# Kernel tuning notes

Hardware: AMD Instinct MI355X
Metric: run time of the kernel (lower is better)

## Reference

```python
import jax, jax.numpy as jnp
import numpy as np

VOCAB = 4096
CODE_DIM = 3


def setup_inputs() -> dict:
    key = jax.random.key(0)
    k1, k2 = jax.random.split(key)
    B, L = 4, 16384
    feats = jax.random.normal(k1, (B, L, CODE_DIM), dtype=jnp.float32)
    # xavier_uniform init for the (vocab, code_dim) embedding table
    limit = float(np.sqrt(6.0 / (VOCAB + CODE_DIM)))
    codebook = jax.random.uniform(k2, (VOCAB, CODE_DIM), dtype=jnp.float32,
                                  minval=-limit, maxval=limit)
    return {"feats": feats, "codebook": codebook}


def reference(feats, codebook):
    """EMAVQ.forward (eval mode): cdist -> argmin -> gather -> vq loss -> straight-through."""
    B, L, D = feats.shape
    flat = feats.reshape(-1, D)                      # (N, D)
    dist = (jnp.sum(flat * flat, axis=1, keepdims=True)
            - 2.0 * (flat @ codebook.T)
            + jnp.sum(codebook * codebook, axis=1))  # (N, V)
    idx = jnp.argmin(dist, axis=1)                   # (N,)
    quant = codebook[idx].reshape(B, L, D)           # embedding gather
    sg = jax.lax.stop_gradient
    loss = (jnp.mean((quant - sg(feats)) ** 2)
            + 0.25 * jnp.mean((feats - sg(quant)) ** 2))
    quant_st = feats + sg(quant - feats)             # straight-through estimator
    return quant_st, idx.reshape(B, L), loss
```

## Files before the change

### kernel.cpp

```cpp
#include <hip/hip_runtime.h>

#define VOCAB 4096
#define SLICES 8
#define SLICE 512
#define GRP 8
#define NGRP (SLICE / GRP)

__device__ __forceinline__ float opaque(float x) {
  asm volatile("" : "+v"(x));
  return x;
}

__device__ __forceinline__ float max3f(float a, float b, float c) {
  float d;
  asm("v_max3_f32 %0, %1, %2, %3" : "=v"(d) : "v"(a), "v"(b), "v"(c));
  return d;
}

__global__ __launch_bounds__(256) void vq_prep_kernel(
    const float* __restrict__ cb, float4* __restrict__ cw,
    float* __restrict__ loss_slot) {
  int j = blockIdx.x * 256 + threadIdx.x;
  if (j == 0) *loss_slot = 0.0f;
  if (j < VOCAB) {
    float e0 = cb[3 * j + 0];
    float e1 = cb[3 * j + 1];
    float e2 = cb[3 * j + 2];
    float p0 = opaque(e0 * e0);
    float p1 = opaque(e1 * e1);
    float p2 = opaque(e2 * e2);
    float c = opaque(opaque(p0 + p1) + p2);
    cw[j] = make_float4(e0, e1, e2, -0.5f * c);
  }
}

__device__ __forceinline__ float tval(float x0, float x1, float x2,
                                      float4 cd) {
  return fmaf(x0, cd.x, fmaf(x1, cd.y, fmaf(x2, cd.z, cd.w)));
}

__device__ __forceinline__ float dist_f32(float x0, float x1, float x2,
                                          float a, float4 cd) {
  float m = fmaf(x2, cd.z, fmaf(x1, cd.y, x0 * cd.x));
  return fmaf(-2.0f, m, a) + (-2.0f * cd.w);
}

__global__ __launch_bounds__(512) void vq_kernel(
    const float* __restrict__ feats, const float4* __restrict__ cw,
    float* __restrict__ out_quant, float* __restrict__ out_idx,
    float* __restrict__ out_loss, int npts) {
  __shared__ float sT1[512];
  __shared__ float sT2[512];
  __shared__ int sG[512];
  __shared__ unsigned long long sSlot[64];
  __shared__ int sList[64];
  __shared__ int sCount;
  __shared__ double sL[64];

  const int tid = threadIdx.x;
  const int lane = tid & 63;
  const int s = __builtin_amdgcn_readfirstlane(tid >> 6);
  const int p = blockIdx.x * 64 + lane;

  if (tid == 0) sCount = 0;

  const float x0 = feats[3 * p + 0];
  const float x1 = feats[3 * p + 1];
  const float x2 = feats[3 * p + 2];

  float xp0 = opaque(x0 * x0);
  float xp1 = opaque(x1 * x1);
  float xp2 = opaque(x2 * x2);
  const float a = opaque(opaque(xp0 + xp1) + xp2);

  const float4* cs = cw + s * SLICE;

  float t1 = -3.4e38f, t2 = -3.4e38f;
  int g1 = 0;
#pragma unroll 2
  for (int g = 0; g < NGRP; ++g) {
    const float4* gp = cs + g * GRP;
    float u0 = tval(x0, x1, x2, gp[0]);
    float u1 = tval(x0, x1, x2, gp[1]);
    float u2 = tval(x0, x1, x2, gp[2]);
    float u3 = tval(x0, x1, x2, gp[3]);
    float u4 = tval(x0, x1, x2, gp[4]);
    float u5 = tval(x0, x1, x2, gp[5]);
    float u6 = tval(x0, x1, x2, gp[6]);
    float u7 = tval(x0, x1, x2, gp[7]);
    float gm = max3f(max3f(u0, u1, u2), max3f(u3, u4, u5), fmaxf(u6, u7));
    t2 = fmaxf(t2, fminf(t1, gm));
    if (gm > t1) g1 = g;
    t1 = fmaxf(t1, gm);
  }
  sT1[tid] = t1;
  sT2[tid] = t2;
  sG[tid] = s * SLICE + g1 * GRP;
  __syncthreads();

  int bi = 0;
  float q0 = 0.0f, q1 = 0.0f, q2 = 0.0f;
  bool flagged = false;
  if (tid < 64) {
    int gbase = sG[tid];
#pragma unroll
    for (int k = 1; k < SLICES; ++k) {
      float b1 = sT1[tid + 64 * k];
      float b2 = sT2[tid + 64 * k];
      t2 = fmaxf(fmaxf(t2, b2), fminf(t1, b1));
      if (b1 > t1) gbase = sG[tid + 64 * k];
      t1 = fmaxf(t1, b1);
    }
    float eps = fmaf(a, 0x1p-21f, 0x1p-20f);
    flagged = !((t1 - t2) > eps);
    if (flagged) {
      int pos = atomicAdd(&sCount, 1);
      sList[pos] = lane;
      sSlot[lane] = ~0ULL;
    } else {
      float bd = 3.4e38f;
#pragma unroll
      for (int k = 0; k < GRP; ++k) {
        float4 cd = cw[gbase + k];
        float d = dist_f32(x0, x1, x2, a, cd);
        if (d < bd) { bd = d; bi = gbase + k; q0 = cd.x; q1 = cd.y; q2 = cd.z; }
      }
    }
  }
  __syncthreads();

  const int cnt = sCount;
  for (int f = 0; f < cnt; ++f) {
    const int fl = sList[f];
    const int fp = blockIdx.x * 64 + fl;
    float y0 = feats[3 * fp + 0];
    float y1 = feats[3 * fp + 1];
    float y2 = feats[3 * fp + 2];
    float yp0 = opaque(y0 * y0);
    float yp1 = opaque(y1 * y1);
    float yp2 = opaque(y2 * y2);
    float ay = opaque(opaque(yp0 + yp1) + yp2);
    float bd = 3.4e38f;
    int bj = 0;
#pragma unroll
    for (int k = 0; k < 8; ++k) {
      float4 cd = cw[tid * 8 + k];
      float d = dist_f32(y0, y1, y2, ay, cd);
      if (d < bd) { bd = d; bj = tid * 8 + k; }
    }
    unsigned b = __float_as_uint(bd);
    b = (b & 0x80000000u) ? ~b : (b | 0x80000000u);
    unsigned long long key = ((unsigned long long)b << 32) | (unsigned)bj;
#pragma unroll
    for (int off = 1; off < 64; off <<= 1) {
      unsigned long long o = __shfl_xor(key, off);
      key = (o < key) ? o : key;
    }
    if (lane == 0) atomicMin(&sSlot[fl], key);
  }
  __syncthreads();

  if (tid < 64) {
    if (flagged) {
      bi = (int)(unsigned)(sSlot[lane] & 0xFFFFFFFFu);
      float4 cd = cw[bi];
      q0 = cd.x; q1 = cd.y; q2 = cd.z;
    }
    float t0 = q0 - x0, t1d = q1 - x1, t2d = q2 - x2;
    out_quant[3 * p + 0] = x0 + t0;
    out_quant[3 * p + 1] = x1 + t1d;
    out_quant[3 * p + 2] = x2 + t2d;
    out_idx[p] = (float)bi;
    sL[lane] = (double)t0 * t0 + (double)t1d * t1d + (double)t2d * t2d;
  }
  __syncthreads();

  if (tid == 0) {
    double acc = 0.0;
#pragma unroll 8
    for (int k = 0; k < 64; ++k) acc += sL[k];
    atomicAdd(out_loss, (float)(acc * (1.25 / ((double)npts * 3.0))));
  }
}

extern "C" void kernel_launch(void* const* d_in, const int* in_sizes, int n_in,
                              void* d_out, int out_size, void* d_ws,
                              size_t ws_size, hipStream_t stream) {
  const float* feats = (const float*)d_in[0];
  const float* cb = (const float*)d_in[1];
  const int npts = in_sizes[0] / 3;

  float* out = (float*)d_out;
  float* out_quant = out;
  float* out_idx = out + in_sizes[0];
  float* out_loss = out + in_sizes[0] + npts;

  float4* cw = (float4*)d_ws;

  vq_prep_kernel<<<VOCAB / 256, 256, 0, stream>>>(cb, cw, out_loss);
  vq_kernel<<<npts / 64, 512, 0, stream>>>(feats, cw, out_quant, out_idx,
                                           out_loss, npts);
}
```

Measured before the change: 108.1 us.

## Stage codebook in LDS and process two points per thread

Each block now copies the whole 4096-entry prepared codebook into shared memory and handles 128 points instead of 64. Every thread scores two points against its codebook slice, so each loaded code entry is reused twice. The aim is to cut codebook fetch and load-issue cost per distance evaluation. In exchange, each block needs about 80KB of LDS, which limits how many blocks fit on a CU, and pays a full codebook copy per block. The wave index is no longer forced to a scalar, so code reads move from scalar loads to LDS broadcast reads.

```diff
diff --git a/kernel.cpp b/kernel.cpp
--- a/kernel.cpp
+++ b/kernel.cpp
@@ -5,6 +5,7 @@
 #define SLICE 512
 #define GRP 8
 #define NGRP (SLICE / GRP)
+#define PTS 128
 
 __device__ __forceinline__ float opaque(float x) {
   asm volatile("" : "+v"(x));
@@ -49,74 +50,100 @@
     const float* __restrict__ feats, const float4* __restrict__ cw,
     float* __restrict__ out_quant, float* __restrict__ out_idx,
     float* __restrict__ out_loss, int npts) {
-  __shared__ float sT1[512];
-  __shared__ float sT2[512];
-  __shared__ int sG[512];
-  __shared__ unsigned long long sSlot[64];
-  __shared__ int sList[64];
+  __shared__ float4 sTab[VOCAB];
+  __shared__ float sT1[SLICES * PTS];
+  __shared__ float sT2[SLICES * PTS];
+  __shared__ int sG[SLICES * PTS];
+  __shared__ unsigned long long sSlot[PTS];
+  __shared__ int sList[PTS];
   __shared__ int sCount;
-  __shared__ double sL[64];
+  __shared__ double sL[PTS];
 
   const int tid = threadIdx.x;
   const int lane = tid & 63;
-  const int s = __builtin_amdgcn_readfirstlane(tid >> 6);
-  const int p = blockIdx.x * 64 + lane;
+  const int s = tid >> 6;
 
   if (tid == 0) sCount = 0;
 
-  const float x0 = feats[3 * p + 0];
-  const float x1 = feats[3 * p + 1];
-  const float x2 = feats[3 * p + 2];
-
-  float xp0 = opaque(x0 * x0);
-  float xp1 = opaque(x1 * x1);
-  float xp2 = opaque(x2 * x2);
-  const float a = opaque(opaque(xp0 + xp1) + xp2);
-
-  const float4* cs = cw + s * SLICE;
-
-  float t1 = -3.4e38f, t2 = -3.4e38f;
-  int g1 = 0;
+#pragma unroll
+  for (int k = 0; k < VOCAB / 512; ++k) sTab[tid + k * 512] = cw[tid + k * 512];
+
+  const int pbase = blockIdx.x * PTS;
+  const int pA = pbase + lane;
+  const int pB = pbase + 64 + lane;
+
+  const float a0 = feats[3 * pA + 0], a1 = feats[3 * pA + 1],
+              a2 = feats[3 * pA + 2];
+  const float b0 = feats[3 * pB + 0], b1 = feats[3 * pB + 1],
+              b2 = feats[3 * pB + 2];
+
+  float ap0 = opaque(a0 * a0), ap1 = opaque(a1 * a1), ap2 = opaque(a2 * a2);
+  const float na = opaque(opaque(ap0 + ap1) + ap2);
+  float bp0 = opaque(b0 * b0), bp1 = opaque(b1 * b1), bp2 = opaque(b2 * b2);
+  const float nb = opaque(opaque(bp0 + bp1) + bp2);
+
+  __syncthreads();
+
+  const float4* cs = sTab + s * SLICE;
+
+  float t1A = -3.4e38f, t2A = -3.4e38f, t1B = -3.4e38f, t2B = -3.4e38f;
+  int gA = 0, gB = 0;
 #pragma unroll 2
   for (int g = 0; g < NGRP; ++g) {
     const float4* gp = cs + g * GRP;
-    float u0 = tval(x0, x1, x2, gp[0]);
-    float u1 = tval(x0, x1, x2, gp[1]);
-    float u2 = tval(x0, x1, x2, gp[2]);
-    float u3 = tval(x0, x1, x2, gp[3]);
-    float u4 = tval(x0, x1, x2, gp[4]);
-    float u5 = tval(x0, x1, x2, gp[5]);
-    float u6 = tval(x0, x1, x2, gp[6]);
-    float u7 = tval(x0, x1, x2, gp[7]);
-    float gm = max3f(max3f(u0, u1, u2), max3f(u3, u4, u5), fmaxf(u6, u7));
-    t2 = fmaxf(t2, fminf(t1, gm));
-    if (gm > t1) g1 = g;
-    t1 = fmaxf(t1, gm);
-  }
-  sT1[tid] = t1;
-  sT2[tid] = t2;
-  sG[tid] = s * SLICE + g1 * GRP;
+    float4 c0 = gp[0], c1 = gp[1], c2 = gp[2], c3 = gp[3];
+    float4 c4 = gp[4], c5 = gp[5], c6 = gp[6], c7 = gp[7];
+    float uA0 = tval(a0, a1, a2, c0), uB0 = tval(b0, b1, b2, c0);
+    float uA1 = tval(a0, a1, a2, c1), uB1 = tval(b0, b1, b2, c1);
+    float uA2 = tval(a0, a1, a2, c2), uB2 = tval(b0, b1, b2, c2);
+    float uA3 = tval(a0, a1, a2, c3), uB3 = tval(b0, b1, b2, c3);
+    float uA4 = tval(a0, a1, a2, c4), uB4 = tval(b0, b1, b2, c4);
+    float uA5 = tval(a0, a1, a2, c5), uB5 = tval(b0, b1, b2, c5);
+    float uA6 = tval(a0, a1, a2, c6), uB6 = tval(b0, b1, b2, c6);
+    float uA7 = tval(a0, a1, a2, c7), uB7 = tval(b0, b1, b2, c7);
+    float gmA = max3f(max3f(uA0, uA1, uA2), max3f(uA3, uA4, uA5),
+                      fmaxf(uA6, uA7));
+    float gmB = max3f(max3f(uB0, uB1, uB2), max3f(uB3, uB4, uB5),
+                      fmaxf(uB6, uB7));
+    t2A = fmaxf(t2A, fminf(t1A, gmA));
+    if (gmA > t1A) gA = g;
+    t1A = fmaxf(t1A, gmA);
+    t2B = fmaxf(t2B, fminf(t1B, gmB));
+    if (gmB > t1B) gB = g;
+    t1B = fmaxf(t1B, gmB);
+  }
+  sT1[s * PTS + lane] = t1A;
+  sT2[s * PTS + lane] = t2A;
+  sG[s * PTS + lane] = s * SLICE + gA * GRP;
+  sT1[s * PTS + 64 + lane] = t1B;
+  sT2[s * PTS + 64 + lane] = t2B;
+  sG[s * PTS + 64 + lane] = s * SLICE + gB * GRP;
   __syncthreads();
 
   int bi = 0;
   float q0 = 0.0f, q1 = 0.0f, q2 = 0.0f;
   bool flagged = false;
-  if (tid < 64) {
+  const float x0 = (s == 0) ? a0 : b0;
+  const float x1 = (s == 0) ? a1 : b1;
+  const float x2 = (s == 0) ? a2 : b2;
+  const float a = (s == 0) ? na : nb;
+  if (tid < PTS) {
+    float t1 = sT1[tid], t2 = sT2[tid];
     int gbase = sG[tid];
 #pragma unroll
     for (int k = 1; k < SLICES; ++k) {
-      float b1 = sT1[tid + 64 * k];
-      float b2 = sT2[tid + 64 * k];
-      t2 = fmaxf(fmaxf(t2, b2), fminf(t1, b1));
-      if (b1 > t1) gbase = sG[tid + 64 * k];
-      t1 = fmaxf(t1, b1);
+      float u1 = sT1[k * PTS + tid];
+      float u2 = sT2[k * PTS + tid];
+      t2 = fmaxf(fmaxf(t2, u2), fminf(t1, u1));
+      if (u1 > t1) gbase = sG[k * PTS + tid];
+      t1 = fmaxf(t1, u1);
     }
     float eps = fmaf(a, 0x1p-21f, 0x1p-20f);
     flagged = !((t1 - t2) > eps);
     if (flagged) {
       int pos = atomicAdd(&sCount, 1);
-      sList[pos] = lane;
-      sSlot[lane] = ~0ULL;
+      sList[pos] = tid;
+      sSlot[tid] = ~0ULL;
     } else {
       float bd = 3.4e38f;
 #pragma unroll
@@ -131,8 +158,8 @@
 
   const int cnt = sCount;
   for (int f = 0; f < cnt; ++f) {
-    const int fl = sList[f];
-    const int fp = blockIdx.x * 64 + fl;
+    const int fpt = sList[f];
+    const int fp = pbase + fpt;
     float y0 = feats[3 * fp + 0];
     float y1 = feats[3 * fp + 1];
     float y2 = feats[3 * fp + 2];
@@ -156,29 +183,30 @@
       unsigned long long o = __shfl_xor(key, off);
       key = (o < key) ? o : key;
     }
-    if (lane == 0) atomicMin(&sSlot[fl], key);
-  }
-  __syncthreads();
-
-  if (tid < 64) {
+    if (lane == 0) atomicMin(&sSlot[fpt], key);
+  }
+  __syncthreads();
+
+  if (tid < PTS) {
     if (flagged) {
-      bi = (int)(unsigned)(sSlot[lane] & 0xFFFFFFFFu);
+      bi = (int)(unsigned)(sSlot[tid] & 0xFFFFFFFFu);
       float4 cd = cw[bi];
       q0 = cd.x; q1 = cd.y; q2 = cd.z;
     }
+    const int p = pbase + tid;
     float t0 = q0 - x0, t1d = q1 - x1, t2d = q2 - x2;
     out_quant[3 * p + 0] = x0 + t0;
     out_quant[3 * p + 1] = x1 + t1d;
     out_quant[3 * p + 2] = x2 + t2d;
     out_idx[p] = (float)bi;
-    sL[lane] = (double)t0 * t0 + (double)t1d * t1d + (double)t2d * t2d;
+    sL[tid] = (double)t0 * t0 + (double)t1d * t1d + (double)t2d * t2d;
   }
   __syncthreads();
 
   if (tid == 0) {
     double acc = 0.0;
 #pragma unroll 8
-    for (int k = 0; k < 64; ++k) acc += sL[k];
+    for (int k = 0; k < PTS; ++k) acc += sL[k];
     atomicAdd(out_loss, (float)(acc * (1.25 / ((double)npts * 3.0))));
   }
 }
@@ -198,6 +226,6 @@
   float4* cw = (float4*)d_ws;
 
   vq_prep_kernel<<<VOCAB / 256, 256, 0, stream>>>(cb, cw, out_loss);
-  vq_kernel<<<npts / 64, 512, 0, stream>>>(feats, cw, out_quant, out_idx,
-                                           out_loss, npts);
-}
+  vq_kernel<<<npts / PTS, 512, 0, stream>>>(feats, cw, out_quant, out_idx,
+                                            out_loss, npts);
+}
```

Measured after the change: 92.78 us. -14.2%, faster.
